# Kernel tuning notes

Hardware: AMD Instinct MI355X
Metric: run time of the kernel (lower is better)

The kernel has to match this reference:

```python
import jax, jax.numpy as jnp
import numpy as np
from jax import lax

B, N, D = 16, 4096, 64
NPOINT, RADIUS, NSAMPLE = 1024, 0.2, 32
MLP = [64, 128, 256]
IN_CH = 3 + D
EPS = 1e-5


def farthest_point_sample(xyz, npoint):
    # Deterministic FPS (start at index 0) matching the python fallback loop.
    b, n, _ = xyz.shape

    def step(carry, _):
        dist, farthest = carry
        centroid = jnp.take_along_axis(xyz, farthest[:, None, None], axis=1)  # [B,1,3]
        d = jnp.sum((xyz - centroid) ** 2, axis=-1)  # [B,N]
        dist = jnp.minimum(dist, d)
        nxt = jnp.argmax(dist, axis=-1)
        return (dist, nxt), farthest

    init = (jnp.full((b, n), 1e10, dtype=xyz.dtype), jnp.zeros((b,), jnp.int32))
    _, idx = lax.scan(step, init, None, length=npoint)
    return idx.T  # [B, npoint]


def index_points(points, idx):
    # points: [B,N,C], idx: [B,S] or [B,S,K]
    return jax.vmap(lambda p, i: p[i])(points, idx)


def square_distance(src, dst):
    # src:[B,S,C], dst:[B,N,C] -> [B,S,N]
    d = -2.0 * jnp.einsum('bsc,bnc->bsn', src, dst)
    d += jnp.sum(src ** 2, -1)[:, :, None]
    d += jnp.sum(dst ** 2, -1)[:, None, :]
    return d


def query_ball_point(radius, nsample, xyz, new_xyz):
    b, n, _ = xyz.shape
    sqrdists = square_distance(new_xyz, xyz)  # [B,S,N]
    group_idx = jnp.where(sqrdists > radius ** 2, n, jnp.arange(n, dtype=jnp.int32))
    group_idx = jnp.sort(group_idx, axis=-1)[:, :, :nsample]  # [B,S,K]
    first = group_idx[:, :, :1]
    return jnp.where(group_idx == n, first, group_idx)


def sample_and_group(npoint, radius, nsample, xyz, points):
    fps_idx = farthest_point_sample(xyz, npoint)
    new_xyz = index_points(xyz, fps_idx)  # [B,S,3]
    idx = query_ball_point(radius, nsample, xyz, new_xyz)  # [B,S,K]
    grouped_xyz = index_points(xyz, idx)  # [B,S,K,3]
    grouped_xyz_norm = grouped_xyz - new_xyz[:, :, None, :]
    grouped_points = index_points(points, idx)  # [B,S,K,D]
    new_points = jnp.concatenate([grouped_xyz_norm, grouped_points], axis=-1)
    return new_xyz, new_points


def setup_inputs() -> dict:
    key = jax.random.key(0)
    ks = jax.random.split(key, 2 + 4 * len(MLP))
    inp = {
        'xyz': jax.random.uniform(ks[0], (B, N, 3), jnp.float32),
        'points': jax.random.normal(ks[1], (B, N, D), jnp.float32),
    }
    last = IN_CH
    for i, out in enumerate(MLP):
        kw, kb = ks[2 + 4 * i], ks[3 + 4 * i]
        scale = 1.0 / np.sqrt(last)
        inp[f'w{i}'] = jax.random.normal(kw, (last, out), jnp.float32) * scale
        inp[f'b{i}'] = jax.random.normal(kb, (out,), jnp.float32) * 0.01
        inp[f'g{i}'] = jnp.ones((out,), jnp.float32)
        inp[f'bt{i}'] = jnp.zeros((out,), jnp.float32)
        last = out
    return inp


def _forward(xyz, points, params):
    new_xyz, x = sample_and_group(NPOINT, RADIUS, NSAMPLE, xyz, points)  # x:[B,S,K,C]
    for w, b, g, bt in params:
        x = jnp.einsum('bskc,cd->bskd', x, w) + b  # 1x1 Conv2d
        mean = jnp.mean(x, axis=(0, 1, 2))
        var = jnp.var(x, axis=(0, 1, 2))  # biased, as torch BN training forward
        x = jax.nn.relu((x - mean) * lax.rsqrt(var + EPS) * g + bt)
    new_points = jnp.max(x, axis=2)  # max over nsample -> [B,S,Cout]
    return new_xyz, new_points


def reference(xyz, points, w0, b0, g0, bt0, w1, b1, g1, bt1, w2, b2, g2, bt2):
    params = [(w0, b0, g0, bt0), (w1, b1, g1, bt1), (w2, b2, g2, bt2)]
    return _forward(xyz, points, params)
```

## Files before the change

### kernel.cpp

```cpp
#include <hip/hip_runtime.h>

namespace {
constexpr int kNB = 16;
constexpr int kN  = 4096;
constexpr int kD  = 64;
constexpr int kS  = 1024;
constexpr int kK  = 32;
constexpr int kG  = kNB * kS;
constexpr int C0 = 67, C1 = 64, C2 = 128, C3 = 256;
constexpr float kEps = 1e-5f;
constexpr double kR2d = 0.04000000000000001;
constexpr float kRowCount = (float)(kG * kK);
constexpr int kFT = 256;
constexpr int kFW = kFT / 64;
constexpr int kFP = kN / kFT;
constexpr int kLS = 33;
constexpr int kXS = 132;
constexpr int kNF = 88;
}

typedef __attribute__((ext_vector_type(8))) short short8;
typedef __attribute__((ext_vector_type(4))) float f32x4;

__device__ __forceinline__ void split_bf16(float x, unsigned& hi, unsigned& lo) {
  const unsigned u = __float_as_uint(x);
  hi = (u + 0x7fffu + ((u >> 16) & 1u)) >> 16;
  const float rem = x - __uint_as_float(hi << 16);
  const unsigned u2 = __float_as_uint(rem);
  lo = ((u2 + 0x7fffu + ((u2 >> 16) & 1u)) >> 16) & 0xffffu;
}
__device__ __forceinline__ unsigned pack_sb(float x) {
  unsigned hi, lo;
  split_bf16(x, hi, lo);
  return (hi << 16) | lo;
}
__device__ __forceinline__ float unpack_sb(unsigned pk) {
  return __uint_as_float(pk & 0xffff0000u) + __uint_as_float(pk << 16);
}

__device__ __forceinline__ f32x4 mfma3(const short8& ah, const short8& al,
                                       const unsigned short* __restrict__ whiF,
                                       const unsigned short* __restrict__ wloF,
                                       size_t fb, f32x4 acc) {
  const short8 bh = *(const short8*)(whiF + fb);
  const short8 bl = *(const short8*)(wloF + fb);
  acc = __builtin_amdgcn_mfma_f32_16x16x32_bf16(ah, bh, acc, 0, 0, 0);
  acc = __builtin_amdgcn_mfma_f32_16x16x32_bf16(ah, bl, acc, 0, 0, 0);
  acc = __builtin_amdgcn_mfma_f32_16x16x32_bf16(al, bh, acc, 0, 0, 0);
  return acc;
}

__device__ __forceinline__ void load_afrag(const unsigned* p, int k0, int mbase,
                                           int quad, int l15, short8& hi, short8& lo) {
#pragma unroll
  for (int j = 0; j < 8; ++j) {
    const unsigned pk = p[(k0 + quad * 8 + j) * kLS + mbase + l15];
    hi[j] = (short)(pk >> 16);
    lo[j] = (short)(pk & 0xffffu);
  }
}

template <int CTRL, int RM>
__device__ __forceinline__ float dpp_max_step(float v) {
  const int vi = __float_as_int(v);
  const int sh = __builtin_amdgcn_update_dpp(vi, vi, CTRL, RM, 0xf, false);
  return fmaxf(v, __int_as_float(sh));
}
__device__ __forceinline__ float wave_max_dpp(float v) {
  v = dpp_max_step<0x111, 0xf>(v);
  v = dpp_max_step<0x112, 0xf>(v);
  v = dpp_max_step<0x114, 0xf>(v);
  v = dpp_max_step<0x118, 0xf>(v);
  v = dpp_max_step<0x142, 0xa>(v);
  v = dpp_max_step<0x143, 0xc>(v);
  return v;
}

__global__ __launch_bounds__(kFT) void fps_kernel(const float* __restrict__ xyz,
                                                  float* __restrict__ new_xyz) {
#pragma clang fp contract(off)
  const int b = blockIdx.x;
  const int tid = threadIdx.x;
  const int w = tid >> 6;
  const int lane = tid & 63;
  const float* xb = xyz + (size_t)b * kN * 3;

  __shared__ float sx[kN], sy[kN], sz[kN];
  __shared__ float sout[kS * 3];
  __shared__ float4 pV[2];
  __shared__ int4   pI[2];

  float px[kFP], py[kFP], pz[kFP], dist[kFP];
#pragma unroll
  for (int j = 0; j < kFP; ++j) {
    const int p = tid * kFP + j;
    const float x = xb[p * 3 + 0];
    const float y = xb[p * 3 + 1];
    const float z = xb[p * 3 + 2];
    px[j] = x; py[j] = y; pz[j] = z;
    sx[p] = x; sy[p] = y; sz[p] = z;
    dist[j] = 1e10f;
  }
  float cx = xb[0], cy = xb[1], cz = xb[2];
  __syncthreads();

  for (int t = 0; t < kS; ++t) {
    if (tid == 0) {
      sout[t * 3 + 0] = cx; sout[t * 3 + 1] = cy; sout[t * 3 + 2] = cz;
    }
    float lv = -1.0f;
    int bi = 0;
#pragma unroll
    for (int j = 0; j < kFP; ++j) {
      const float dx = px[j] - cx, dy = py[j] - cy, dz = pz[j] - cz;
      float d = dx * dx + dy * dy;
      d = d + dz * dz;
      const float dd = fminf(dist[j], d);
      dist[j] = dd;
      if (dd > lv) { lv = dd; bi = tid * kFP + j; }
    }
    const float wm = wave_max_dpp(lv);
    const float sM = __int_as_float(__builtin_amdgcn_readlane(__float_as_int(wm), 63));
    const unsigned long long mk = __ballot(lv == sM);
    const int fl = __builtin_ctzll(mk);
    const int cand = __builtin_amdgcn_readlane(bi, fl);
    const int par = t & 1;
    if (lane == 0) {
      ((float*)&pV[par])[w] = sM;
      ((int*)&pI[par])[w] = cand;
    }
    __syncthreads();
    const float4 vv = pV[par];
    const int4 ii = pI[par];
    float bv = vv.x; int bci = ii.x;
    if (vv.y > bv) { bv = vv.y; bci = ii.y; }
    if (vv.z > bv) { bv = vv.z; bci = ii.z; }
    if (vv.w > bv) { bv = vv.w; bci = ii.w; }
    cx = sx[bci]; cy = sy[bci]; cz = sz[bci];
  }
  __syncthreads();
  float* ob = new_xyz + (size_t)b * kS * 3;
  for (int e = tid; e < kS * 3; e += kFT) ob[e] = sout[e];
}

__global__ __launch_bounds__(256) void ball_kernel(const float* __restrict__ xyz,
                                                   const float* __restrict__ new_xyz,
                                                   int* __restrict__ idx) {
  const int g = blockIdx.x * 4 + (threadIdx.x >> 6);
  const int lane = threadIdx.x & 63;
  const int b = g >> 10;
  const float* xb = xyz + (size_t)b * kN * 3;
  const double sx = (double)new_xyz[(size_t)g * 3 + 0];
  const double sy = (double)new_xyz[(size_t)g * 3 + 1];
  const double sz = (double)new_xyz[(size_t)g * 3 + 2];
  const double s2 = sx * sx + sy * sy + sz * sz;
  int have = 0, first = -1;
  int* out = idx + (size_t)g * kK;
  for (int c = 0; c < kN; c += 64) {
    const int p = c + lane;
    const double px = (double)xb[p * 3 + 0];
    const double py = (double)xb[p * 3 + 1];
    const double pz = (double)xb[p * 3 + 2];
    const double p2 = px * px + py * py + pz * pz;
    const double dot = sx * px + sy * py + sz * pz;
    const double d = -2.0 * dot + s2 + p2;
    const bool elig = !(d > kR2d);
    const unsigned long long mask = __ballot(elig);
    if (first < 0 && mask) first = c + __builtin_ctzll(mask);
    const int pos = have + __popcll(mask & ((1ull << lane) - 1ull));
    if (elig && pos < kK) out[pos] = p;
    have += __popcll(mask);
    if (have >= kK) break;
  }
  if (have < kK) {
    if (lane >= have && lane < kK) out[lane] = first;
  }
}

__global__ __launch_bounds__(256) void wsplit_kernel(const float* __restrict__ w0,
                                                     const float* __restrict__ w1,
                                                     const float* __restrict__ w2,
                                                     unsigned short* __restrict__ whiF,
                                                     unsigned short* __restrict__ wloF) {
  const int gid = blockIdx.x * 256 + threadIdx.x;
  const int lane = gid & 63;
  const int f = gid >> 6;
  const int quad = lane >> 4, l15 = lane & 15;
  const float* src;
  int kt, nt, nstride;
  if (f < 8) { src = w0; kt = f >> 2; nt = f & 3; nstride = C1; }
  else if (f < 24) { const int fl = f - 8; src = w1; kt = fl >> 3; nt = fl & 7; nstride = C2; }
  else { const int fl = f - 24; src = w2; kt = fl >> 4; nt = fl & 15; nstride = C3; }
  const int k0 = kt * 32 + quad * 8;
  const int n = nt * 16 + l15;
#pragma unroll
  for (int j = 0; j < 8; ++j) {
    const float x = src[(size_t)(k0 + j) * nstride + n];
    unsigned hi, lo;
    split_bf16(x, hi, lo);
    whiF[(size_t)gid * 8 + j] = (unsigned short)hi;
    wloF[(size_t)gid * 8 + j] = (unsigned short)lo;
  }
}

__device__ __forceinline__ void gather_packed(int g, const float* __restrict__ xyz,
                                              const float* __restrict__ points,
                                              const float* __restrict__ new_xyz,
                                              const int* __restrict__ idx,
                                              unsigned* fsp) {
  const int b = g >> 10;
  const float* xb = xyz + (size_t)b * kN * 3;
  const float* pb = points + (size_t)b * kN * kD;
  const int* ig = idx + (size_t)g * kK;
  const int tid = threadIdx.x;
#pragma unroll
  for (int it = 0; it < 2; ++it) {
    const int e = tid + it * 256;
    const int r = e >> 4, c4 = e & 15;
    const int i = ig[r];
    const float4 v = *(const float4*)(pb + (size_t)i * kD + c4 * 4);
    const int cb = 3 + c4 * 4;
    fsp[(cb + 0) * kLS + r] = pack_sb(v.x);
    fsp[(cb + 1) * kLS + r] = pack_sb(v.y);
    fsp[(cb + 2) * kLS + r] = pack_sb(v.z);
    fsp[(cb + 3) * kLS + r] = pack_sb(v.w);
  }
  if (tid < 96) {
    const int c = tid >> 5, r = tid & 31;
    const int i = ig[r];
    const float v = xb[i * 3 + c] - new_xyz[(size_t)g * 3 + c];
    fsp[c * kLS + r] = pack_sb(v);
  }
}

__device__ __forceinline__ void l1_mfma(const unsigned* fsp,
                                        const unsigned short* __restrict__ whiF,
                                        const unsigned short* __restrict__ wloF,
                                        const float* __restrict__ w0,
                                        const float* __restrict__ b0,
                                        int mt, int nh, int quad, int l15, int lane,
                                        f32x4 out[2]) {
  short8 ah[2], al[2];
#pragma unroll
  for (int ks = 0; ks < 2; ++ks)
    load_afrag(fsp, ks * 32, mt * 16, quad, l15, ah[ks], al[ks]);
#pragma unroll
  for (int nt2 = 0; nt2 < 2; ++nt2) {
    const int nt = nh * 2 + nt2;
    const int n = nt * 16 + l15;
    f32x4 acc = {0.f, 0.f, 0.f, 0.f};
#pragma unroll
    for (int ks = 0; ks < 2; ++ks)
      acc = mfma3(ah[ks], al[ks], whiF, wloF, ((size_t)(ks * 4 + nt) * 64 + lane) * 8, acc);
#pragma unroll
    for (int c = 64; c < 67; ++c) {
      const float wv0 = w0[(size_t)c * C1 + n];
#pragma unroll
      for (int r = 0; r < 4; ++r) {
        const float x = unpack_sb(fsp[c * kLS + mt * 16 + quad * 4 + r]);
        acc[r] += x * wv0;
      }
    }
    const float bb = b0[n];
#pragma unroll
    for (int r = 0; r < 4; ++r) acc[r] += bb;
    out[nt2] = acc;
  }
}

__global__ __launch_bounds__(256) void stats1_kernel(
    const float* __restrict__ xyz, const float* __restrict__ points,
    const float* __restrict__ new_xyz, const int* __restrict__ idx,
    const float* __restrict__ w0, const float* __restrict__ b0,
    const unsigned short* __restrict__ whiF, const unsigned short* __restrict__ wloF,
    float* __restrict__ P) {
  __shared__ unsigned fsp[C0 * kLS];
  __shared__ float redS[C1 * 2], redQ[C1 * 2];
  const int g = blockIdx.x;
  const int tid = threadIdx.x;
  gather_packed(g, xyz, points, new_xyz, idx, fsp);
  __syncthreads();
  const int wv = tid >> 6, lane = tid & 63;
  const int mt = wv & 1, nh = wv >> 1;
  const int quad = lane >> 4, l15 = lane & 15;
  f32x4 acc1[2];
  l1_mfma(fsp, whiF, wloF, w0, b0, mt, nh, quad, l15, lane, acc1);
#pragma unroll
  for (int nt2 = 0; nt2 < 2; ++nt2) {
    const int n = (nh * 2 + nt2) * 16 + l15;
    const f32x4 a = acc1[nt2];
    float s = a[0] + a[1] + a[2] + a[3];
    float q = a[0] * a[0] + a[1] * a[1] + a[2] * a[2] + a[3] * a[3];
    s += __shfl_xor(s, 16); s += __shfl_xor(s, 32);
    q += __shfl_xor(q, 16); q += __shfl_xor(q, 32);
    if (quad == 0) { redS[n * 2 + mt] = s; redQ[n * 2 + mt] = q; }
  }
  __syncthreads();
  if (tid < C1) {
    P[(size_t)g * 2 * C1 + tid] = redS[tid * 2] + redS[tid * 2 + 1];
    P[(size_t)g * 2 * C1 + C1 + tid] = redQ[tid * 2] + redQ[tid * 2 + 1];
  }
}

__global__ __launch_bounds__(256) void stats2_kernel(
    const float* __restrict__ xyz, const float* __restrict__ points,
    const float* __restrict__ new_xyz, const int* __restrict__ idx,
    const float* __restrict__ w0, const float* __restrict__ b0, const float* __restrict__ ab0,
    const float* __restrict__ b1,
    const unsigned short* __restrict__ whiF, const unsigned short* __restrict__ wloF,
    float* __restrict__ P, unsigned* __restrict__ x2p) {
  __shared__ unsigned fsp[C0 * kLS];
  __shared__ unsigned y1p[C1 * kLS];
  __shared__ unsigned x2s[32 * kXS];
  __shared__ float redS[C2 * 2], redQ[C2 * 2];
  const int g = blockIdx.x;
  const int tid = threadIdx.x;
  gather_packed(g, xyz, points, new_xyz, idx, fsp);
  __syncthreads();
  const int wv = tid >> 6, lane = tid & 63;
  const int mt = wv & 1, nh = wv >> 1;
  const int quad = lane >> 4, l15 = lane & 15;
  {
    f32x4 acc1[2];
    l1_mfma(fsp, whiF, wloF, w0, b0, mt, nh, quad, l15, lane, acc1);
#pragma unroll
    for (int nt2 = 0; nt2 < 2; ++nt2) {
      const int n = (nh * 2 + nt2) * 16 + l15;
      const float a = ab0[n * 2 + 0], c = ab0[n * 2 + 1];
#pragma unroll
      for (int r = 0; r < 4; ++r) {
        const float y = fmaxf(acc1[nt2][r] * a + c, 0.f);
        y1p[n * kLS + mt * 16 + quad * 4 + r] = pack_sb(y);
      }
    }
  }
  __syncthreads();
  {
    short8 ah[2], al[2];
#pragma unroll
    for (int ks = 0; ks < 2; ++ks)
      load_afrag(y1p, ks * 32, mt * 16, quad, l15, ah[ks], al[ks]);
#pragma unroll
    for (int nt2 = 0; nt2 < 4; ++nt2) {
      const int nt = nh * 4 + nt2;
      const int n = nt * 16 + l15;
      f32x4 acc = {0.f, 0.f, 0.f, 0.f};
#pragma unroll
      for (int ks = 0; ks < 2; ++ks)
        acc = mfma3(ah[ks], al[ks], whiF, wloF, ((size_t)(8 + ks * 8 + nt) * 64 + lane) * 8, acc);
      const float bb = b1[n];
      const float v0 = acc[0] + bb, v1 = acc[1] + bb, v2 = acc[2] + bb, v3 = acc[3] + bb;
      if (x2p) {
        const int m0 = mt * 16 + quad * 4;
        x2s[(m0 + 0) * kXS + n] = pack_sb(v0);
        x2s[(m0 + 1) * kXS + n] = pack_sb(v1);
        x2s[(m0 + 2) * kXS + n] = pack_sb(v2);
        x2s[(m0 + 3) * kXS + n] = pack_sb(v3);
      }
      float s = v0 + v1 + v2 + v3;
      float q = v0 * v0 + v1 * v1 + v2 * v2 + v3 * v3;
      s += __shfl_xor(s, 16); s += __shfl_xor(s, 32);
      q += __shfl_xor(q, 16); q += __shfl_xor(q, 32);
      if (quad == 0) { redS[n * 2 + mt] = s; redQ[n * 2 + mt] = q; }
    }
  }
  __syncthreads();
  if (x2p) {
#pragma unroll
    for (int i = 0; i < 16; ++i) {
      const int f = tid + i * 256;
      const int m = f >> 7, n = f & 127;
      x2p[(size_t)g * 4096 + f] = x2s[m * kXS + n];
    }
  }
  if (tid < C2) {
    P[(size_t)g * 2 * C2 + tid] = redS[tid * 2] + redS[tid * 2 + 1];
    P[(size_t)g * 2 * C2 + C2 + tid] = redQ[tid * 2] + redQ[tid * 2 + 1];
  }
}

__global__ __launch_bounds__(256) void stats3_kernel(
    const float* __restrict__ xyz, const float* __restrict__ points,
    const float* __restrict__ new_xyz, const int* __restrict__ idx,
    const float* __restrict__ w0, const float* __restrict__ b0, const float* __restrict__ ab0,
    const float* __restrict__ b1, const float* __restrict__ ab1,
    const float* __restrict__ b2,
    const unsigned short* __restrict__ whiF, const unsigned short* __restrict__ wloF,
    float* __restrict__ P, float* __restrict__ maxv, float* __restrict__ minv) {
  __shared__ unsigned fsp[C0 * kLS];
  __shared__ unsigned y1p[C1 * kLS];
  __shared__ unsigned y2p[C2 * kLS];
  __shared__ float redS[C3 * 2], redQ[C3 * 2], redM[C3 * 2], redN[C3 * 2];
  const int g = blockIdx.x;
  const int tid = threadIdx.x;
  gather_packed(g, xyz, points, new_xyz, idx, fsp);
  __syncthreads();
  const int wv = tid >> 6, lane = tid & 63;
  const int mt = wv & 1, nh = wv >> 1;
  const int quad = lane >> 4, l15 = lane & 15;
  {
    f32x4 acc1[2];
    l1_mfma(fsp, whiF, wloF, w0, b0, mt, nh, quad, l15, lane, acc1);
#pragma unroll
    for (int nt2 = 0; nt2 < 2; ++nt2) {
      const int n = (nh * 2 + nt2) * 16 + l15;
      const float a = ab0[n * 2 + 0], c = ab0[n * 2 + 1];
#pragma unroll
      for (int r = 0; r < 4; ++r) {
        const float y = fmaxf(acc1[nt2][r] * a + c, 0.f);
        y1p[n * kLS + mt * 16 + quad * 4 + r] = pack_sb(y);
      }
    }
  }
  __syncthreads();
  {
    short8 ah[2], al[2];
#pragma unroll
    for (int ks = 0; ks < 2; ++ks)
      load_afrag(y1p, ks * 32, mt * 16, quad, l15, ah[ks], al[ks]);
#pragma unroll
    for (int nt2 = 0; nt2 < 4; ++nt2) {
      const int nt = nh * 4 + nt2;
      const int n = nt * 16 + l15;
      f32x4 acc = {0.f, 0.f, 0.f, 0.f};
#pragma unroll
      for (int ks = 0; ks < 2; ++ks)
        acc = mfma3(ah[ks], al[ks], whiF, wloF, ((size_t)(8 + ks * 8 + nt) * 64 + lane) * 8, acc);
      const float bb = b1[n];
      const float a = ab1[n * 2 + 0], c = ab1[n * 2 + 1];
#pragma unroll
      for (int r = 0; r < 4; ++r) {
        const float y = fmaxf((acc[r] + bb) * a + c, 0.f);
        y2p[n * kLS + mt * 16 + quad * 4 + r] = pack_sb(y);
      }
    }
  }
  __syncthreads();
  {
    short8 ah[4], al[4];
#pragma unroll
    for (int ks = 0; ks < 4; ++ks)
      load_afrag(y2p, ks * 32, mt * 16, quad, l15, ah[ks], al[ks]);
#pragma unroll
    for (int nt2 = 0; nt2 < 8; ++nt2) {
      const int nt = nh * 8 + nt2;
      f32x4 acc = {0.f, 0.f, 0.f, 0.f};
#pragma unroll
      for (int ks = 0; ks < 4; ++ks)
        acc = mfma3(ah[ks], al[ks], whiF, wloF, ((size_t)(24 + ks * 16 + nt) * 64 + lane) * 8, acc);
      const int n = nt * 16 + l15;
      const float bn = b2[n];
      const float v0 = acc[0] + bn, v1 = acc[1] + bn, v2 = acc[2] + bn, v3 = acc[3] + bn;
      float s = v0 + v1 + v2 + v3;
      float q = v0 * v0 + v1 * v1 + v2 * v2 + v3 * v3;
      float mx = fmaxf(fmaxf(v0, v1), fmaxf(v2, v3));
      float mn = fminf(fminf(v0, v1), fminf(v2, v3));
      s += __shfl_xor(s, 16); s += __shfl_xor(s, 32);
      q += __shfl_xor(q, 16); q += __shfl_xor(q, 32);
      mx = fmaxf(mx, __shfl_xor(mx, 16)); mx = fmaxf(mx, __shfl_xor(mx, 32));
      mn = fminf(mn, __shfl_xor(mn, 16)); mn = fminf(mn, __shfl_xor(mn, 32));
      if (quad == 0) {
        redS[n * 2 + mt] = s; redQ[n * 2 + mt] = q;
        redM[n * 2 + mt] = mx; redN[n * 2 + mt] = mn;
      }
    }
  }
  __syncthreads();
  {
    const int ch = tid;
    P[(size_t)g * 2 * C3 + ch] = redS[ch * 2] + redS[ch * 2 + 1];
    P[(size_t)g * 2 * C3 + C3 + ch] = redQ[ch * 2] + redQ[ch * 2 + 1];
    maxv[(size_t)g * C3 + ch] = fmaxf(redM[ch * 2], redM[ch * 2 + 1]);
    minv[(size_t)g * C3 + ch] = fminf(redN[ch * 2], redN[ch * 2 + 1]);
  }
}

__global__ __launch_bounds__(256) void stats3p_kernel(
    const unsigned* __restrict__ x2p, const float* __restrict__ ab1,
    const float* __restrict__ b2,
    const unsigned short* __restrict__ whiF, const unsigned short* __restrict__ wloF,
    float* __restrict__ P, float* __restrict__ maxv, float* __restrict__ minv) {
  __shared__ unsigned y2p[C2 * kLS];
  __shared__ float sab[2 * C2];
  __shared__ float redS[C3 * 2], redQ[C3 * 2], redM[C3 * 2], redN[C3 * 2];
  const int g = blockIdx.x;
  const int tid = threadIdx.x;
  sab[tid] = ab1[tid];
  __syncthreads();
#pragma unroll
  for (int i = 0; i < 16; ++i) {
    const int f = tid + i * 256;
    const int m = f >> 7, n = f & 127;
    const unsigned pk = x2p[(size_t)g * 4096 + f];
    const float x = unpack_sb(pk);
    const float y = fmaxf(x * sab[n * 2 + 0] + sab[n * 2 + 1], 0.f);
    y2p[n * kLS + m] = pack_sb(y);
  }
  __syncthreads();
  const int wv = tid >> 6, lane = tid & 63;
  const int mt = wv & 1, nh = wv >> 1;
  const int quad = lane >> 4, l15 = lane & 15;
  {
    short8 ah[4], al[4];
#pragma unroll
    for (int ks = 0; ks < 4; ++ks)
      load_afrag(y2p, ks * 32, mt * 16, quad, l15, ah[ks], al[ks]);
#pragma unroll
    for (int nt2 = 0; nt2 < 8; ++nt2) {
      const int nt = nh * 8 + nt2;
      f32x4 acc = {0.f, 0.f, 0.f, 0.f};
#pragma unroll
      for (int ks = 0; ks < 4; ++ks)
        acc = mfma3(ah[ks], al[ks], whiF, wloF, ((size_t)(24 + ks * 16 + nt) * 64 + lane) * 8, acc);
      const int n = nt * 16 + l15;
      const float bn = b2[n];
      const float v0 = acc[0] + bn, v1 = acc[1] + bn, v2 = acc[2] + bn, v3 = acc[3] + bn;
      float s = v0 + v1 + v2 + v3;
      float q = v0 * v0 + v1 * v1 + v2 * v2 + v3 * v3;
      float mx = fmaxf(fmaxf(v0, v1), fmaxf(v2, v3));
      float mn = fminf(fminf(v0, v1), fminf(v2, v3));
      s += __shfl_xor(s, 16); s += __shfl_xor(s, 32);
      q += __shfl_xor(q, 16); q += __shfl_xor(q, 32);
      mx = fmaxf(mx, __shfl_xor(mx, 16)); mx = fmaxf(mx, __shfl_xor(mx, 32));
      mn = fminf(mn, __shfl_xor(mn, 16)); mn = fminf(mn, __shfl_xor(mn, 32));
      if (quad == 0) {
        redS[n * 2 + mt] = s; redQ[n * 2 + mt] = q;
        redM[n * 2 + mt] = mx; redN[n * 2 + mt] = mn;
      }
    }
  }
  __syncthreads();
  {
    const int ch = tid;
    P[(size_t)g * 2 * C3 + ch] = redS[ch * 2] + redS[ch * 2 + 1];
    P[(size_t)g * 2 * C3 + C3 + ch] = redQ[ch * 2] + redQ[ch * 2 + 1];
    maxv[(size_t)g * C3 + ch] = fmaxf(redM[ch * 2], redM[ch * 2 + 1]);
    minv[(size_t)g * C3 + ch] = fminf(redN[ch * 2], redN[ch * 2 + 1]);
  }
}

__global__ __launch_bounds__(256) void reduce_kernel(const float* __restrict__ P, int CH,
                                                     const float* __restrict__ gamma,
                                                     const float* __restrict__ beta,
                                                     float* __restrict__ ab) {
  const int ch = blockIdx.x;
  float s = 0.f, q = 0.f;
  for (int i = threadIdx.x; i < kG; i += 256) {
    s += P[(size_t)i * 2 * CH + ch];
    q += P[(size_t)i * 2 * CH + CH + ch];
  }
#pragma unroll
  for (int off = 32; off > 0; off >>= 1) {
    s += __shfl_down(s, off);
    q += __shfl_down(q, off);
  }
  __shared__ float ss[4], qs[4];
  if ((threadIdx.x & 63) == 0) { ss[threadIdx.x >> 6] = s; qs[threadIdx.x >> 6] = q; }
  __syncthreads();
  if (threadIdx.x == 0) {
    s = ss[0] + ss[1] + ss[2] + ss[3];
    q = qs[0] + qs[1] + qs[2] + qs[3];
    const float mean = s / kRowCount;
    float var = q / kRowCount - mean * mean;
    var = fmaxf(var, 0.f);
    const float a = gamma[ch] * (1.0f / sqrtf(var + kEps));
    const float c = beta[ch] - mean * a;
    ab[ch * 2 + 0] = a;
    ab[ch * 2 + 1] = c;
  }
}

__global__ __launch_bounds__(256) void final_kernel(const float* __restrict__ ab2,
                                                    const float* __restrict__ maxv,
                                                    const float* __restrict__ minv,
                                                    float* __restrict__ out) {
  const int e = blockIdx.x * 256 + threadIdx.x;
  const int ch = e & (C3 - 1);
  const float a = ab2[ch * 2 + 0];
  const float c = ab2[ch * 2 + 1];
  const float m = (a >= 0.f) ? maxv[e] : minv[e];
  out[e] = fmaxf(a * m + c, 0.f);
}

extern "C" void kernel_launch(void* const* d_in, const int* in_sizes, int n_in,
                              void* d_out, int out_size, void* d_ws, size_t ws_size,
                              hipStream_t stream) {
  const float* xyz = (const float*)d_in[0];
  const float* points = (const float*)d_in[1];
  const float* w0 = (const float*)d_in[2];
  const float* b0 = (const float*)d_in[3];
  const float* g0 = (const float*)d_in[4];
  const float* bt0 = (const float*)d_in[5];
  const float* w1 = (const float*)d_in[6];
  const float* b1 = (const float*)d_in[7];
  const float* g1 = (const float*)d_in[8];
  const float* bt1 = (const float*)d_in[9];
  const float* w2 = (const float*)d_in[10];
  const float* b2 = (const float*)d_in[11];
  const float* g2 = (const float*)d_in[12];
  const float* bt2 = (const float*)d_in[13];

  float* out_xyz = (float*)d_out;
  float* out_pts = out_xyz + (size_t)kG * 3;

  char* ws = (char*)d_ws;
  int* idx = (int*)ws;
  float* P = (float*)(ws + (size_t)kG * kK * sizeof(int));
  float* maxv = P + (size_t)kG * 2 * C3;
  float* minv = maxv + (size_t)kG * C3;
  float* ab0 = minv + (size_t)kG * C3;
  float* ab1 = ab0 + 2 * C1;
  float* ab2 = ab1 + 2 * C2;
  unsigned short* whiF = (unsigned short*)(ab2 + 2 * C3);
  unsigned short* wloF = whiF + (size_t)kNF * 512;
  unsigned* x2p = (unsigned*)(wloF + (size_t)kNF * 512);
  const size_t needed = (size_t)((char*)(x2p + (size_t)kG * 4096) - ws);
  const bool persist = ws_size >= needed;
  unsigned* x2arg = persist ? x2p : nullptr;

  wsplit_kernel<<<kNF / 4, 256, 0, stream>>>(w0, w1, w2, whiF, wloF);
  fps_kernel<<<kNB, kFT, 0, stream>>>(xyz, out_xyz);
  ball_kernel<<<kG / 4, 256, 0, stream>>>(xyz, out_xyz, idx);
  stats1_kernel<<<kG, 256, 0, stream>>>(xyz, points, out_xyz, idx, w0, b0, whiF, wloF, P);
  reduce_kernel<<<C1, 256, 0, stream>>>(P, C1, g0, bt0, ab0);
  stats2_kernel<<<kG, 256, 0, stream>>>(xyz, points, out_xyz, idx, w0, b0, ab0, b1,
                                        whiF, wloF, P, x2arg);
  reduce_kernel<<<C2, 256, 0, stream>>>(P, C2, g1, bt1, ab1);
  if (persist) {
    stats3p_kernel<<<kG, 256, 0, stream>>>(x2p, ab1, b2, whiF, wloF, P, maxv, minv);
  } else {
    stats3_kernel<<<kG, 256, 0, stream>>>(xyz, points, out_xyz, idx, w0, b0, ab0,
                                          b1, ab1, b2, whiF, wloF, P, maxv, minv);
  }
  reduce_kernel<<<C3, 256, 0, stream>>>(P, C3, g2, bt2, ab2);
  final_kernel<<<(kG * C3) / 256, 256, 0, stream>>>(ab2, maxv, minv, out_pts);
}
```

Baseline: 1.296 ms.

## Persist layer-1 activations and widen FPS block to 512 threads

The FPS kernel now uses 512 threads with 8 waves, stores coordinates as packed float4 in shared memory, and reduces eight per-wave candidates per step. Stats1 now writes the pre-BN layer-1 outputs, packed as bf16 hi/lo pairs, to workspace. When the workspace is large enough, stats2 reads those values back instead of redoing the gather and the first MFMA layer. This trades recomputation for extra global memory traffic (about 128 MB written and read) and depends on the workspace size.

```diff
diff --git a/kernel.cpp b/kernel.cpp
--- a/kernel.cpp
+++ b/kernel.cpp
@@ -11,11 +11,12 @@
 constexpr float kEps = 1e-5f;
 constexpr double kR2d = 0.04000000000000001;
 constexpr float kRowCount = (float)(kG * kK);
-constexpr int kFT = 256;
+constexpr int kFT = 512;
 constexpr int kFW = kFT / 64;
 constexpr int kFP = kN / kFT;
 constexpr int kLS = 33;
 constexpr int kXS = 132;
+constexpr int kX1S = 66;
 constexpr int kNF = 88;
 }
 
@@ -85,10 +86,10 @@
   const int lane = tid & 63;
   const float* xb = xyz + (size_t)b * kN * 3;
 
-  __shared__ float sx[kN], sy[kN], sz[kN];
+  __shared__ float4 sxyz[kN];
   __shared__ float sout[kS * 3];
-  __shared__ float4 pV[2];
-  __shared__ int4   pI[2];
+  __shared__ __align__(16) float pV[2][kFW];
+  __shared__ __align__(16) int   pI[2][kFW];
 
   float px[kFP], py[kFP], pz[kFP], dist[kFP];
 #pragma unroll
@@ -98,7 +99,7 @@
     const float y = xb[p * 3 + 1];
     const float z = xb[p * 3 + 2];
     px[j] = x; py[j] = y; pz[j] = z;
-    sx[p] = x; sy[p] = y; sz[p] = z;
+    sxyz[p] = make_float4(x, y, z, 0.f);
     dist[j] = 1e10f;
   }
   float cx = xb[0], cy = xb[1], cz = xb[2];
@@ -125,18 +126,22 @@
     const int fl = __builtin_ctzll(mk);
     const int cand = __builtin_amdgcn_readlane(bi, fl);
     const int par = t & 1;
-    if (lane == 0) {
-      ((float*)&pV[par])[w] = sM;
-      ((int*)&pI[par])[w] = cand;
-    }
+    if (lane == 0) { pV[par][w] = sM; pI[par][w] = cand; }
     __syncthreads();
-    const float4 vv = pV[par];
-    const int4 ii = pI[par];
-    float bv = vv.x; int bci = ii.x;
-    if (vv.y > bv) { bv = vv.y; bci = ii.y; }
-    if (vv.z > bv) { bv = vv.z; bci = ii.z; }
-    if (vv.w > bv) { bv = vv.w; bci = ii.w; }
-    cx = sx[bci]; cy = sy[bci]; cz = sz[bci];
+    const float4 v0 = *(const float4*)&pV[par][0];
+    const float4 v1 = *(const float4*)&pV[par][4];
+    const int4 i0 = *(const int4*)&pI[par][0];
+    const int4 i1 = *(const int4*)&pI[par][4];
+    float bv = v0.x; int bci = i0.x;
+    if (v0.y > bv) { bv = v0.y; bci = i0.y; }
+    if (v0.z > bv) { bv = v0.z; bci = i0.z; }
+    if (v0.w > bv) { bv = v0.w; bci = i0.w; }
+    if (v1.x > bv) { bv = v1.x; bci = i1.x; }
+    if (v1.y > bv) { bv = v1.y; bci = i1.y; }
+    if (v1.z > bv) { bv = v1.z; bci = i1.z; }
+    if (v1.w > bv) { bv = v1.w; bci = i1.w; }
+    const float4 c = sxyz[bci];
+    cx = c.x; cy = c.y; cz = c.z;
   }
   __syncthreads();
   float* ob = new_xyz + (size_t)b * kS * 3;
@@ -273,8 +278,9 @@
     const float* __restrict__ new_xyz, const int* __restrict__ idx,
     const float* __restrict__ w0, const float* __restrict__ b0,
     const unsigned short* __restrict__ whiF, const unsigned short* __restrict__ wloF,
-    float* __restrict__ P) {
+    float* __restrict__ P, unsigned* __restrict__ x1p) {
   __shared__ unsigned fsp[C0 * kLS];
+  __shared__ unsigned x1s[32 * kX1S];
   __shared__ float redS[C1 * 2], redQ[C1 * 2];
   const int g = blockIdx.x;
   const int tid = threadIdx.x;
@@ -289,6 +295,13 @@
   for (int nt2 = 0; nt2 < 2; ++nt2) {
     const int n = (nh * 2 + nt2) * 16 + l15;
     const f32x4 a = acc1[nt2];
+    if (x1p) {
+      const int m0 = mt * 16 + quad * 4;
+      x1s[(m0 + 0) * kX1S + n] = pack_sb(a[0]);
+      x1s[(m0 + 1) * kX1S + n] = pack_sb(a[1]);
+      x1s[(m0 + 2) * kX1S + n] = pack_sb(a[2]);
+      x1s[(m0 + 3) * kX1S + n] = pack_sb(a[3]);
+    }
     float s = a[0] + a[1] + a[2] + a[3];
     float q = a[0] * a[0] + a[1] * a[1] + a[2] * a[2] + a[3] * a[3];
     s += __shfl_xor(s, 16); s += __shfl_xor(s, 32);
@@ -296,6 +309,14 @@
     if (quad == 0) { redS[n * 2 + mt] = s; redQ[n * 2 + mt] = q; }
   }
   __syncthreads();
+  if (x1p) {
+#pragma unroll
+    for (int i = 0; i < 8; ++i) {
+      const int f = tid + i * 256;
+      const int m = f >> 6, n = f & 63;
+      x1p[(size_t)g * 2048 + f] = x1s[m * kX1S + n];
+    }
+  }
   if (tid < C1) {
     P[(size_t)g * 2 * C1 + tid] = redS[tid * 2] + redS[tid * 2 + 1];
     P[(size_t)g * 2 * C1 + C1 + tid] = redQ[tid * 2] + redQ[tid * 2 + 1];
@@ -308,19 +329,31 @@
     const float* __restrict__ w0, const float* __restrict__ b0, const float* __restrict__ ab0,
     const float* __restrict__ b1,
     const unsigned short* __restrict__ whiF, const unsigned short* __restrict__ wloF,
-    float* __restrict__ P, unsigned* __restrict__ x2p) {
+    float* __restrict__ P, const unsigned* __restrict__ x1p, unsigned* __restrict__ x2p) {
   __shared__ unsigned fsp[C0 * kLS];
   __shared__ unsigned y1p[C1 * kLS];
   __shared__ unsigned x2s[32 * kXS];
+  __shared__ float sab0[2 * C1];
   __shared__ float redS[C2 * 2], redQ[C2 * 2];
   const int g = blockIdx.x;
   const int tid = threadIdx.x;
-  gather_packed(g, xyz, points, new_xyz, idx, fsp);
-  __syncthreads();
   const int wv = tid >> 6, lane = tid & 63;
   const int mt = wv & 1, nh = wv >> 1;
   const int quad = lane >> 4, l15 = lane & 15;
-  {
+  if (x1p) {
+    if (tid < 2 * C1) sab0[tid] = ab0[tid];
+    __syncthreads();
+#pragma unroll
+    for (int i = 0; i < 8; ++i) {
+      const int f = tid + i * 256;
+      const int m = f >> 6, n = f & 63;
+      const float x = unpack_sb(x1p[(size_t)g * 2048 + f]);
+      const float y = fmaxf(x * sab0[n * 2 + 0] + sab0[n * 2 + 1], 0.f);
+      y1p[n * kLS + m] = pack_sb(y);
+    }
+  } else {
+    gather_packed(g, xyz, points, new_xyz, idx, fsp);
+    __syncthreads();
     f32x4 acc1[2];
     l1_mfma(fsp, whiF, wloF, w0, b0, mt, nh, quad, l15, lane, acc1);
 #pragma unroll
@@ -614,17 +647,22 @@
   unsigned short* whiF = (unsigned short*)(ab2 + 2 * C3);
   unsigned short* wloF = whiF + (size_t)kNF * 512;
   unsigned* x2p = (unsigned*)(wloF + (size_t)kNF * 512);
-  const size_t needed = (size_t)((char*)(x2p + (size_t)kG * 4096) - ws);
-  const bool persist = ws_size >= needed;
+  unsigned* x1p = x2p + (size_t)kG * 4096;
+  const size_t needed1 = (size_t)((char*)(x2p + (size_t)kG * 4096) - ws);
+  const size_t needed2 = (size_t)((char*)(x1p + (size_t)kG * 2048) - ws);
+  const bool persist = ws_size >= needed1;
+  const bool persist2 = ws_size >= needed2;
   unsigned* x2arg = persist ? x2p : nullptr;
+  unsigned* x1arg = persist2 ? x1p : nullptr;
 
   wsplit_kernel<<<kNF / 4, 256, 0, stream>>>(w0, w1, w2, whiF, wloF);
   fps_kernel<<<kNB, kFT, 0, stream>>>(xyz, out_xyz);
   ball_kernel<<<kG / 4, 256, 0, stream>>>(xyz, out_xyz, idx);
-  stats1_kernel<<<kG, 256, 0, stream>>>(xyz, points, out_xyz, idx, w0, b0, whiF, wloF, P);
+  stats1_kernel<<<kG, 256, 0, stream>>>(xyz, points, out_xyz, idx, w0, b0, whiF, wloF,
+                                        P, x1arg);
   reduce_kernel<<<C1, 256, 0, stream>>>(P, C1, g0, bt0, ab0);
   stats2_kernel<<<kG, 256, 0, stream>>>(xyz, points, out_xyz, idx, w0, b0, ab0, b1,
-                                        whiF, wloF, P, x2arg);
+                                        whiF, wloF, P, x1arg, x2arg);
   reduce_kernel<<<C2, 256, 0, stream>>>(P, C2, g1, bt1, ab1);
   if (persist) {
     stats3p_kernel<<<kG, 256, 0, stream>>>(x2p, ab1, b2, whiF, wloF, P, maxv, minv);
```

New measurement: 1.383 ms. 6.7% more time.
